# Performance work log

Measured on AMD Instinct MI355X. Metric: run time of the kernel, lower is better.

The kernel has to match this reference:

```python
import jax, jax.numpy as jnp
import numpy as np

B, N, D, H, O = 4096, 128, 64, 256, 128  # batch, memory_size, memory_dim, controller_dim, output_size


def setup_inputs() -> dict:
    key = jax.random.key(0)
    ks = jax.random.split(key, 20)
    s = 0.05
    inp = {
        "x": jax.random.normal(ks[0], (B, O), jnp.float32),
        "memory": jax.random.normal(ks[1], (B, N, D), jnp.float32),
        "h": jax.random.normal(ks[2], (B, H), jnp.float32),
        "c": jax.random.normal(ks[3], (B, H), jnp.float32),
        # LSTMCell params (torch layout: gates ordered i, f, g, o; input = x||read_vec of width O+D)
        "W_ih": jax.random.normal(ks[4], (4 * H, O + D), jnp.float32) * s,
        "W_hh": jax.random.normal(ks[5], (4 * H, H), jnp.float32) * s,
        "b_ih": jax.random.normal(ks[6], (4 * H,), jnp.float32) * s,
        "b_hh": jax.random.normal(ks[7], (4 * H,), jnp.float32) * s,
        "W_read": jax.random.normal(ks[8], (N, H), jnp.float32) * s,
        "b_read": jax.random.normal(ks[9], (N,), jnp.float32) * s,
        "W_write": jax.random.normal(ks[10], (N, H), jnp.float32) * s,
        "b_write": jax.random.normal(ks[11], (N,), jnp.float32) * s,
        "W_erase": jax.random.normal(ks[12], (D, H), jnp.float32) * s,
        "b_erase": jax.random.normal(ks[13], (D,), jnp.float32) * s,
        "W_add": jax.random.normal(ks[14], (D, H), jnp.float32) * s,
        "b_add": jax.random.normal(ks[15], (D,), jnp.float32) * s,
        "W_out": jax.random.normal(ks[16], (O, H + D), jnp.float32) * s,
        "b_out": jax.random.normal(ks[17], (O,), jnp.float32) * s,
    }
    return inp


def reference(x, memory, h, c, W_ih, W_hh, b_ih, b_hh, W_read, b_read,
              W_write, b_write, W_erase, b_erase, W_add, b_add, W_out, b_out):
    # read: softmax attention over memory rows, addressed by previous hidden state
    read_w = jax.nn.softmax(h @ W_read.T + b_read, axis=-1)          # [B, N]
    read_vec = jnp.einsum("bn,bnd->bd", read_w, memory)               # [B, D]

    # LSTMCell step (torch gate order: i, f, g, o)
    ctrl_in = jnp.concatenate([x, read_vec], axis=-1)                 # [B, O+D]
    gates = ctrl_in @ W_ih.T + b_ih + h @ W_hh.T + b_hh               # [B, 4H]
    i, f, g, o = jnp.split(gates, 4, axis=-1)
    i, f, o = jax.nn.sigmoid(i), jax.nn.sigmoid(f), jax.nn.sigmoid(o)
    g = jnp.tanh(g)
    c_new = f * c + i * g
    h_new = o * jnp.tanh(c_new)

    # write: outer-product erase/add update
    write_w = jax.nn.softmax(h_new @ W_write.T + b_write, axis=-1)    # [B, N]
    erase = jax.nn.sigmoid(h_new @ W_erase.T + b_erase)               # [B, D]
    add = jnp.tanh(h_new @ W_add.T + b_add)                           # [B, D]
    ww = write_w[:, :, None]                                          # [B, N, 1]
    mem_new = memory * (1.0 - ww * erase[:, None, :]) + ww * add[:, None, :]

    out = jnp.concatenate([h_new, read_vec], axis=-1) @ W_out.T + b_out  # [B, O]
    return (out, mem_new, h_new, c_new)
```

## Files before the change

### kernel.cpp

```cpp
#include <hip/hip_runtime.h>
#include <math.h>


typedef __attribute__((ext_vector_type(8))) short bf16x8;
typedef __attribute__((ext_vector_type(4))) float f32x4;
typedef __attribute__((ext_vector_type(4))) unsigned short us4;

#define MFMA16(a, b, c) __builtin_amdgcn_mfma_f32_16x16x32_bf16(a, b, c, 0, 0, 0)
#define GLL16(gp, lp) __builtin_amdgcn_global_load_lds( \
    (const __attribute__((address_space(1))) void*)(gp), \
    (__attribute__((address_space(3))) void*)(lp), 16, 0, 0)
#define SW(row, s) ((s) ^ ((row) & 3))

__device__ __forceinline__ float sigf(float v) { return 1.f / (1.f + __expf(-v)); }

__device__ __forceinline__ unsigned short f2bf(float f) {
    unsigned u = __builtin_bit_cast(unsigned, f);
    u = (u + 0x7FFFu + ((u >> 16) & 1u)) >> 16;
    return (unsigned short)u;
}

__device__ __forceinline__ int swA8(int r, int c) {
    return r * 320 + (c & ~31) + ((((c >> 3) & 3) ^ (r & 3)) << 3) + (c & 7);
}

__global__ __launch_bounds__(256) void kA_scores(
    const float* __restrict__ h, const float* __restrict__ Wr,
    const float* __restrict__ br, float* __restrict__ read_w)
{
    __shared__ unsigned short As[16 * 32];
    __shared__ unsigned short Bs[128 * 32];
    __shared__ float sc[16][128];

    int t = threadIdx.x;
    int wid = t >> 6, lane = t & 63;
    int cl = lane & 15, ks = lane >> 4;
    int b0 = blockIdx.x * 16;

    int aOff = cl * 32 + SW(cl, ks) * 8;
    int bOff[4];
#pragma unroll
    for (int f = 0; f < 4; ++f) {
        int br_ = (wid * 4 + f) * 16 + cl;
        bOff[f] = br_ * 32 + SW(br_, ks) * 8;
    }
    f32x4 acc[4] = {};
    for (int kc = 0; kc < 8; ++kc) {
        __syncthreads();
        {
            int row = t >> 4, k0 = (t & 15) * 2;
            float2 hv = *(const float2*)(h + (size_t)(b0 + row) * 256 + kc * 32 + k0);
            unsigned pk = (unsigned)f2bf(hv.x) | ((unsigned)f2bf(hv.y) << 16);
            *(unsigned*)(As + row * 32 + SW(row, k0 >> 3) * 8 + (k0 & 7)) = pk;
        }
        {
            int row = t >> 1, k0 = (t & 1) * 16;
            const float4* wp = (const float4*)(Wr + (size_t)row * 256 + kc * 32 + k0);
            float4 w0 = wp[0], w1 = wp[1], w2 = wp[2], w3 = wp[3];
            us4 p0 = { f2bf(w0.x), f2bf(w0.y), f2bf(w0.z), f2bf(w0.w) };
            us4 p1 = { f2bf(w1.x), f2bf(w1.y), f2bf(w1.z), f2bf(w1.w) };
            us4 p2 = { f2bf(w2.x), f2bf(w2.y), f2bf(w2.z), f2bf(w2.w) };
            us4 p3 = { f2bf(w3.x), f2bf(w3.y), f2bf(w3.z), f2bf(w3.w) };
            int g0 = k0 >> 3;
            unsigned short* basep = Bs + row * 32;
            *(us4*)(basep + SW(row, g0) * 8)         = p0;
            *(us4*)(basep + SW(row, g0) * 8 + 4)     = p1;
            *(us4*)(basep + SW(row, g0 + 1) * 8)     = p2;
            *(us4*)(basep + SW(row, g0 + 1) * 8 + 4) = p3;
        }
        __syncthreads();
        if (wid < 2) {
            bf16x8 a = *(const bf16x8*)(As + aOff);
#pragma unroll
            for (int f = 0; f < 4; ++f)
                acc[f] = MFMA16(a, *(const bf16x8*)(Bs + bOff[f]), acc[f]);
        }
    }
    if (wid < 2) {
#pragma unroll
        for (int f = 0; f < 4; ++f)
#pragma unroll
            for (int r = 0; r < 4; ++r)
                sc[ks * 4 + r][(wid * 4 + f) * 16 + cl] = acc[f][r];
    }
    __syncthreads();
    {
        int row = t >> 4, l = t & 15;
        float v[8];
#pragma unroll
        for (int j = 0; j < 8; ++j) v[j] = sc[row][l + 16 * j] + br[l + 16 * j];
        float m = v[0];
#pragma unroll
        for (int j = 1; j < 8; ++j) m = fmaxf(m, v[j]);
#pragma unroll
        for (int mk = 8; mk >= 1; mk >>= 1) m = fmaxf(m, __shfl_xor(m, mk));
        float s = 0.f;
#pragma unroll
        for (int j = 0; j < 8; ++j) { v[j] = __expf(v[j] - m); s += v[j]; }
#pragma unroll
        for (int mk = 8; mk >= 1; mk >>= 1) s += __shfl_xor(s, mk);
        float inv = 1.f / s;
#pragma unroll
        for (int j = 0; j < 8; ++j)
            read_w[(size_t)(b0 + row) * 128 + l + 16 * j] = v[j] * inv;
    }
}

__global__ __launch_bounds__(256) void k2_stream_pack(
    const float* __restrict__ mem, const float* __restrict__ read_w,
    const float* __restrict__ x, const float* __restrict__ h,
    const float* __restrict__ Wih, const float* __restrict__ Whh,
    const float* __restrict__ bih, const float* __restrict__ bhh,
    const float* __restrict__ Ww, const float* __restrict__ We,
    const float* __restrict__ Wa, const float* __restrict__ bw,
    const float* __restrict__ be, const float* __restrict__ ba,
    const float* __restrict__ Wo,
    unsigned short* __restrict__ Wg, unsigned short* __restrict__ Wh_b,
    unsigned short* __restrict__ Wo_b, float* __restrict__ bsum,
    float* __restrict__ bh_b, unsigned short* __restrict__ Ag,
    unsigned short* __restrict__ Aout)
{
    __shared__ float part[16][68];
    int t = threadIdx.x;
    int b = blockIdx.x;
    unsigned idx = b * 256 + t;

    if (idx < 458752) {
        int r = idx / 448, cc = idx - r * 448;
        float v = (cc < 192) ? Wih[(size_t)r * 192 + cc] : Whh[(size_t)r * 256 + (cc - 192)];
        Wg[idx] = f2bf(v);
    }
    if (idx < 65536) {
        int r = idx >> 8, cc = idx & 255;
        float v = (r < 128) ? Ww[(size_t)r * 256 + cc]
                : (r < 192) ? We[(size_t)(r - 128) * 256 + cc]
                            : Wa[(size_t)(r - 192) * 256 + cc];
        Wh_b[idx] = f2bf(v);
    }
    if (idx < 40960) Wo_b[idx] = f2bf(Wo[idx]);
    if (idx < 1024)  bsum[idx] = bih[idx] + bhh[idx];
    if (idx < 256)
        bh_b[idx] = (idx < 128) ? bw[idx] : (idx < 192 ? be[idx - 128] : ba[idx - 192]);

    if (t < 96) {
        int j = t;
        float4 v = (j < 32) ? ((const float4*)(x + (size_t)b * 128))[j]
                            : ((const float4*)(h + (size_t)b * 256))[j - 32];
        us4 o = { f2bf(v.x), f2bf(v.y), f2bf(v.z), f2bf(v.w) };
        int col = (j < 32) ? j * 4 : 192 + (j - 32) * 4;
        *(us4*)(Ag + (size_t)b * 448 + col) = o;
    }

    int np = t >> 4, d4 = t & 15;
    const float4* m4 = (const float4*)(mem + (size_t)b * 8192);
    float4 acc = make_float4(0.f, 0.f, 0.f, 0.f);
#pragma unroll
    for (int j = 0; j < 8; ++j) {
        int n = np + 16 * j;
        float w = read_w[(size_t)b * 128 + n];
        float4 mv = m4[t + 256 * j];
        acc.x += w * mv.x; acc.y += w * mv.y; acc.z += w * mv.z; acc.w += w * mv.w;
    }
    part[np][d4 * 4 + 0] = acc.x; part[np][d4 * 4 + 1] = acc.y;
    part[np][d4 * 4 + 2] = acc.z; part[np][d4 * 4 + 3] = acc.w;
    __syncthreads();
    if (t < 64) {
        float s = 0.f;
#pragma unroll
        for (int q = 0; q < 16; ++q) s += part[q][t];
        unsigned short bv = f2bf(s);
        Ag[(size_t)b * 448 + 128 + t] = bv;
        Aout[(size_t)b * 320 + 256 + t] = bv;
    }
}

__global__ __launch_bounds__(256) void kB_gates(
    const unsigned short* __restrict__ Ag, const unsigned short* __restrict__ Wg,
    const float* __restrict__ bsum, const float* __restrict__ c,
    float* __restrict__ h_new, float* __restrict__ c_new,
    unsigned short* __restrict__ Aout)
{
    __shared__ unsigned short As[32 * 64];
    __shared__ unsigned short Bs[256 * 64];
    int t = threadIdx.x;
    int wid = t >> 6, lane = t & 63;
    int cl = lane & 15, ks = lane >> 4;
    int b0 = blockIdx.x * 32;
    int u0 = blockIdx.y * 64;

    int arow = t >> 3, aseg = t & 7;
    const unsigned short* aSrc = Ag + (size_t)(b0 + arow) * 448 + ((aseg ^ (arow & 7)) * 8);
    unsigned short* aDst = As + t * 8;
    const unsigned short* bSrc[8];
    unsigned short* bDst[8];
#pragma unroll
    for (int j = 0; j < 8; ++j) {
        int i = j * 256 + t;
        int rl = i >> 3, seg = i & 7;
        int g = rl >> 6, u = rl & 63;
        bSrc[j] = Wg + (size_t)(g * 256 + u0 + u) * 448 + ((seg ^ (rl & 7)) * 8);
        bDst[j] = Bs + i * 8;
    }

    int aOff[2][2];
#pragma unroll
    for (int rf = 0; rf < 2; ++rf)
#pragma unroll
        for (int kk = 0; kk < 2; ++kk) {
            int mr = rf * 16 + cl;
            aOff[rf][kk] = mr * 64 + (((kk * 4 + ks) ^ (cl & 7)) * 8);
        }
    int bOff[4][2];
#pragma unroll
    for (int g = 0; g < 4; ++g)
#pragma unroll
        for (int kk = 0; kk < 2; ++kk) {
            int br_ = g * 64 + wid * 16 + cl;
            bOff[g][kk] = br_ * 64 + (((kk * 4 + ks) ^ (cl & 7)) * 8);
        }

    f32x4 acc[2][4] = {};
    for (int kc = 0; kc < 7; ++kc) {
        __syncthreads();
        GLL16(aSrc, aDst);
#pragma unroll
        for (int j = 0; j < 8; ++j) GLL16(bSrc[j], bDst[j]);
        aSrc += 64;
#pragma unroll
        for (int j = 0; j < 8; ++j) bSrc[j] += 64;
        __syncthreads();
#pragma unroll
        for (int kk = 0; kk < 2; ++kk) {
            bf16x8 a[2], b[4];
#pragma unroll
            for (int rf = 0; rf < 2; ++rf) a[rf] = *(const bf16x8*)(As + aOff[rf][kk]);
#pragma unroll
            for (int g = 0; g < 4; ++g) b[g] = *(const bf16x8*)(Bs + bOff[g][kk]);
#pragma unroll
            for (int rf = 0; rf < 2; ++rf)
#pragma unroll
                for (int g = 0; g < 4; ++g)
                    acc[rf][g] = MFMA16(a[rf], b[g], acc[rf][g]);
        }
    }

    int unit = u0 + wid * 16 + cl;
    float bi = bsum[unit], bf_ = bsum[256 + unit];
    float bg = bsum[512 + unit], bo_ = bsum[768 + unit];
#pragma unroll
    for (int rf = 0; rf < 2; ++rf) {
#pragma unroll
        for (int r = 0; r < 4; ++r) {
            int row = b0 + rf * 16 + ks * 4 + r;
            float iv = sigf(acc[rf][0][r] + bi);
            float fv = sigf(acc[rf][1][r] + bf_);
            float gv = tanhf(acc[rf][2][r] + bg);
            float ov = sigf(acc[rf][3][r] + bo_);
            float cv = fv * c[(size_t)row * 256 + unit] + iv * gv;
            float hv = ov * tanhf(cv);
            c_new[(size_t)row * 256 + unit] = cv;
            h_new[(size_t)row * 256 + unit] = hv;
            Aout[(size_t)row * 320 + unit] = f2bf(hv);
        }
    }
}

__global__ __launch_bounds__(256) void kC_heads_out(
    const unsigned short* __restrict__ Aout, const unsigned short* __restrict__ Wh_b,
    const unsigned short* __restrict__ Wo_b, const float* __restrict__ bh_b,
    const float* __restrict__ bo, float* __restrict__ write_w,
    float* __restrict__ erase, float* __restrict__ addv, float* __restrict__ outp)
{
    __shared__ unsigned short As8[8 * 320];
    __shared__ unsigned short Bh[256 * 32];
    __shared__ unsigned short Bo[128 * 32];
    __shared__ float sc8[8][256];

    int t = threadIdx.x;
    int wid = t >> 6, lane = t & 63;
    int cl = lane & 15, ks = lane >> 4;
    int r0 = blockIdx.x * 8;

    for (int i = t; i < 640; i += 256) {
        int row = i / 80, c4 = (i - row * 80) * 4;
        us4 v = *(const us4*)(Aout + (size_t)(r0 + row) * 320 + c4);
        *(us4*)(As8 + swA8(row, c4)) = v;
    }

    const unsigned short* bhSrc[4];
    unsigned short* bhDst[4];
#pragma unroll
    for (int j = 0; j < 4; ++j) {
        int rl = (j * 256 + t) >> 2;
        bhSrc[j] = Wh_b + (size_t)rl * 256 + SW(rl, t & 3) * 8;
        bhDst[j] = Bh + (j * 256 + wid * 64) * 8;
    }
    const unsigned short* boSrc[2];
    unsigned short* boDst[2];
#pragma unroll
    for (int j = 0; j < 2; ++j) {
        int rj = j * 64 + (t >> 2);
        boSrc[j] = Wo_b + (size_t)rj * 320 + SW(rj, t & 3) * 8;
        boDst[j] = Bo + j * 2048 + wid * 512;
    }

    int bOffH[4], bOffO[2];
#pragma unroll
    for (int j = 0; j < 4; ++j) { int br_ = (wid + 4 * j) * 16 + cl; bOffH[j] = br_ * 32 + SW(br_, ks) * 8; }
#pragma unroll
    for (int j = 0; j < 2; ++j) { int br_ = (wid + 4 * j) * 16 + cl; bOffO[j] = br_ * 32 + SW(br_, ks) * 8; }

    f32x4 accH[4] = {};
    f32x4 accO[2] = {};
    for (int kc = 0; kc < 10; ++kc) {
        __syncthreads();
        if (kc < 8) {
            GLL16(bhSrc[0], bhDst[0]); GLL16(bhSrc[1], bhDst[1]);
            GLL16(bhSrc[2], bhDst[2]); GLL16(bhSrc[3], bhDst[3]);
#pragma unroll
            for (int j = 0; j < 4; ++j) bhSrc[j] += 32;
        }
        GLL16(boSrc[0], boDst[0]); GLL16(boSrc[1], boDst[1]);
#pragma unroll
        for (int j = 0; j < 2; ++j) boSrc[j] += 32;
        __syncthreads();
        bf16x8 a = *(const bf16x8*)(As8 + swA8(cl & 7, kc * 32 + ks * 8));
        if (kc < 8) {
#pragma unroll
            for (int j = 0; j < 4; ++j)
                accH[j] = MFMA16(a, *(const bf16x8*)(Bh + bOffH[j]), accH[j]);
        }
#pragma unroll
        for (int j = 0; j < 2; ++j)
            accO[j] = MFMA16(a, *(const bf16x8*)(Bo + bOffO[j]), accO[j]);
    }

    if (ks < 2) {
#pragma unroll
        for (int j = 0; j < 4; ++j) {
            int col = (wid + 4 * j) * 16 + cl;
            float bb = bh_b[col];
#pragma unroll
            for (int r = 0; r < 4; ++r) sc8[ks * 4 + r][col] = accH[j][r] + bb;
        }
#pragma unroll
        for (int j = 0; j < 2; ++j) {
            int ocol = (wid + 4 * j) * 16 + cl;
            float bb = bo[ocol];
#pragma unroll
            for (int r = 0; r < 4; ++r)
                outp[(size_t)(r0 + ks * 4 + r) * 128 + ocol] = accO[j][r] + bb;
        }
    }
    __syncthreads();

    if (t < 128) {
        int row = t >> 4, l = t & 15;
        float v[8];
#pragma unroll
        for (int j = 0; j < 8; ++j) v[j] = sc8[row][l + 16 * j];
        float m = v[0];
#pragma unroll
        for (int j = 1; j < 8; ++j) m = fmaxf(m, v[j]);
#pragma unroll
        for (int mk = 8; mk >= 1; mk >>= 1) m = fmaxf(m, __shfl_xor(m, mk));
        float s = 0.f;
#pragma unroll
        for (int j = 0; j < 8; ++j) { v[j] = __expf(v[j] - m); s += v[j]; }
#pragma unroll
        for (int mk = 8; mk >= 1; mk >>= 1) s += __shfl_xor(s, mk);
        float inv = 1.f / s;
        int row_g = r0 + row;
#pragma unroll
        for (int j = 0; j < 8; ++j)
            write_w[(size_t)row_g * 128 + l + 16 * j] = v[j] * inv;
#pragma unroll
        for (int j = 0; j < 4; ++j)
            erase[(size_t)row_g * 64 + l + 16 * j] = sigf(sc8[row][128 + l + 16 * j]);
#pragma unroll
        for (int j = 0; j < 4; ++j)
            addv[(size_t)row_g * 64 + l + 16 * j] = tanhf(sc8[row][192 + l + 16 * j]);
    }
}

__global__ __launch_bounds__(256) void k5_mem_update(
    const float* __restrict__ mem, const float* __restrict__ write_w,
    const float* __restrict__ erase, const float* __restrict__ addv,
    float* __restrict__ mem_new)
{
    int t = threadIdx.x; int b = blockIdx.x;
    int np = t >> 4, d0 = (t & 15) * 4;
    const f32x4* m4 = (const f32x4*)(mem + (size_t)b * 8192);
    f32x4* o4 = (f32x4*)(mem_new + (size_t)b * 8192);
    f32x4 e4 = *(const f32x4*)(erase + (size_t)b * 64 + d0);
    f32x4 a4 = *(const f32x4*)(addv + (size_t)b * 64 + d0);
#pragma unroll
    for (int j = 0; j < 8; ++j) {
        int n = np + 16 * j;
        float w = write_w[(size_t)b * 128 + n];
        f32x4 m = m4[t + 256 * j];
        f32x4 r;
        r[0] = m[0] * (1.f - w * e4[0]) + w * a4[0];
        r[1] = m[1] * (1.f - w * e4[1]) + w * a4[1];
        r[2] = m[2] * (1.f - w * e4[2]) + w * a4[2];
        r[3] = m[3] * (1.f - w * e4[3]) + w * a4[3];
        __builtin_nontemporal_store(r, &o4[t + 256 * j]);
    }
}

extern "C" void kernel_launch(void* const* d_in, const int* in_sizes, int n_in,
                              void* d_out, int out_size, void* d_ws, size_t ws_size,
                              hipStream_t stream)
{
    const float* x    = (const float*)d_in[0];
    const float* mem  = (const float*)d_in[1];
    const float* h    = (const float*)d_in[2];
    const float* c    = (const float*)d_in[3];
    const float* Wih  = (const float*)d_in[4];
    const float* Whh  = (const float*)d_in[5];
    const float* bih  = (const float*)d_in[6];
    const float* bhh  = (const float*)d_in[7];
    const float* Wr   = (const float*)d_in[8];
    const float* br   = (const float*)d_in[9];
    const float* Ww   = (const float*)d_in[10];
    const float* bw   = (const float*)d_in[11];
    const float* We   = (const float*)d_in[12];
    const float* be   = (const float*)d_in[13];
    const float* Wa   = (const float*)d_in[14];
    const float* ba   = (const float*)d_in[15];
    const float* Wo   = (const float*)d_in[16];
    const float* bo   = (const float*)d_in[17];

    float* out     = (float*)d_out;
    float* mem_new = out + 524288;
    float* h_new   = out + 34078720;
    float* c_new   = out + 35127296;

    float* ws      = (float*)d_ws;
    float* read_w  = ws;
    float* write_w = ws + 524288;
    float* erase   = ws + 1048576;
    float* addv    = ws + 1310720;
    float* bsum    = ws + 1572864;
    float* bh_b    = ws + 1573888;
    unsigned short* ub   = (unsigned short*)(ws + 1574144);
    unsigned short* Ag   = ub;
    unsigned short* Aout = ub + 1835008;
    unsigned short* Wg   = ub + 3145728;
    unsigned short* Wh_b = ub + 3604480;
    unsigned short* Wo_b = ub + 3670016;

    kA_scores<<<256, 256, 0, stream>>>(h, Wr, br, read_w);
    k2_stream_pack<<<4096, 256, 0, stream>>>(mem, read_w, x, h, Wih, Whh, bih, bhh,
                                             Ww, We, Wa, bw, be, ba, Wo,
                                             Wg, Wh_b, Wo_b, bsum, bh_b, Ag, Aout);
    kB_gates<<<dim3(128, 4), 256, 0, stream>>>(Ag, Wg, bsum, c, h_new, c_new, Aout);
    kC_heads_out<<<512, 256, 0, stream>>>(Aout, Wh_b, Wo_b, bh_b, bo,
                                          write_w, erase, addv, out);
    k5_mem_update<<<4096, 256, 0, stream>>>(mem, write_w, erase, addv, mem_new);
}
```

Baseline: 103.3 us.

## Fuse read-score GEMV and softmax into memory streaming kernel

```diff
diff --git a/kernel.cpp b/kernel.cpp
--- a/kernel.cpp
+++ b/kernel.cpp
@@ -24,93 +24,12 @@
     return r * 320 + (c & ~31) + ((((c >> 3) & 3) ^ (r & 3)) << 3) + (c & 7);
 }
 
-__global__ __launch_bounds__(256) void kA_scores(
-    const float* __restrict__ h, const float* __restrict__ Wr,
-    const float* __restrict__ br, float* __restrict__ read_w)
-{
-    __shared__ unsigned short As[16 * 32];
-    __shared__ unsigned short Bs[128 * 32];
-    __shared__ float sc[16][128];
-
-    int t = threadIdx.x;
-    int wid = t >> 6, lane = t & 63;
-    int cl = lane & 15, ks = lane >> 4;
-    int b0 = blockIdx.x * 16;
-
-    int aOff = cl * 32 + SW(cl, ks) * 8;
-    int bOff[4];
-#pragma unroll
-    for (int f = 0; f < 4; ++f) {
-        int br_ = (wid * 4 + f) * 16 + cl;
-        bOff[f] = br_ * 32 + SW(br_, ks) * 8;
-    }
-    f32x4 acc[4] = {};
-    for (int kc = 0; kc < 8; ++kc) {
-        __syncthreads();
-        {
-            int row = t >> 4, k0 = (t & 15) * 2;
-            float2 hv = *(const float2*)(h + (size_t)(b0 + row) * 256 + kc * 32 + k0);
-            unsigned pk = (unsigned)f2bf(hv.x) | ((unsigned)f2bf(hv.y) << 16);
-            *(unsigned*)(As + row * 32 + SW(row, k0 >> 3) * 8 + (k0 & 7)) = pk;
-        }
-        {
-            int row = t >> 1, k0 = (t & 1) * 16;
-            const float4* wp = (const float4*)(Wr + (size_t)row * 256 + kc * 32 + k0);
-            float4 w0 = wp[0], w1 = wp[1], w2 = wp[2], w3 = wp[3];
-            us4 p0 = { f2bf(w0.x), f2bf(w0.y), f2bf(w0.z), f2bf(w0.w) };
-            us4 p1 = { f2bf(w1.x), f2bf(w1.y), f2bf(w1.z), f2bf(w1.w) };
-            us4 p2 = { f2bf(w2.x), f2bf(w2.y), f2bf(w2.z), f2bf(w2.w) };
-            us4 p3 = { f2bf(w3.x), f2bf(w3.y), f2bf(w3.z), f2bf(w3.w) };
-            int g0 = k0 >> 3;
-            unsigned short* basep = Bs + row * 32;
-            *(us4*)(basep + SW(row, g0) * 8)         = p0;
-            *(us4*)(basep + SW(row, g0) * 8 + 4)     = p1;
-            *(us4*)(basep + SW(row, g0 + 1) * 8)     = p2;
-            *(us4*)(basep + SW(row, g0 + 1) * 8 + 4) = p3;
-        }
-        __syncthreads();
-        if (wid < 2) {
-            bf16x8 a = *(const bf16x8*)(As + aOff);
-#pragma unroll
-            for (int f = 0; f < 4; ++f)
-                acc[f] = MFMA16(a, *(const bf16x8*)(Bs + bOff[f]), acc[f]);
-        }
-    }
-    if (wid < 2) {
-#pragma unroll
-        for (int f = 0; f < 4; ++f)
-#pragma unroll
-            for (int r = 0; r < 4; ++r)
-                sc[ks * 4 + r][(wid * 4 + f) * 16 + cl] = acc[f][r];
-    }
-    __syncthreads();
-    {
-        int row = t >> 4, l = t & 15;
-        float v[8];
-#pragma unroll
-        for (int j = 0; j < 8; ++j) v[j] = sc[row][l + 16 * j] + br[l + 16 * j];
-        float m = v[0];
-#pragma unroll
-        for (int j = 1; j < 8; ++j) m = fmaxf(m, v[j]);
-#pragma unroll
-        for (int mk = 8; mk >= 1; mk >>= 1) m = fmaxf(m, __shfl_xor(m, mk));
-        float s = 0.f;
-#pragma unroll
-        for (int j = 0; j < 8; ++j) { v[j] = __expf(v[j] - m); s += v[j]; }
-#pragma unroll
-        for (int mk = 8; mk >= 1; mk >>= 1) s += __shfl_xor(s, mk);
-        float inv = 1.f / s;
-#pragma unroll
-        for (int j = 0; j < 8; ++j)
-            read_w[(size_t)(b0 + row) * 128 + l + 16 * j] = v[j] * inv;
-    }
-}
-
 __global__ __launch_bounds__(256) void k2_stream_pack(
-    const float* __restrict__ mem, const float* __restrict__ read_w,
+    const float* __restrict__ mem,
     const float* __restrict__ x, const float* __restrict__ h,
     const float* __restrict__ Wih, const float* __restrict__ Whh,
     const float* __restrict__ bih, const float* __restrict__ bhh,
+    const float* __restrict__ Wr, const float* __restrict__ br,
     const float* __restrict__ Ww, const float* __restrict__ We,
     const float* __restrict__ Wa, const float* __restrict__ bw,
     const float* __restrict__ be, const float* __restrict__ ba,
@@ -121,6 +40,8 @@
     unsigned short* __restrict__ Aout)
 {
     __shared__ float part[16][68];
+    __shared__ float scr[128];
+    __shared__ float wL[128];
     int t = threadIdx.x;
     int b = blockIdx.x;
     unsigned idx = b * 256 + t;
@@ -151,13 +72,42 @@
         *(us4*)(Ag + (size_t)b * 448 + col) = o;
     }
 
+    {
+        int w = t >> 6, l = t & 63;
+        float4 hv = ((const float4*)(h + (size_t)b * 256))[l];
+#pragma unroll 4
+        for (int i = 0; i < 32; ++i) {
+            int n = w * 32 + i;
+            float4 wv = ((const float4*)(Wr + (size_t)n * 256))[l];
+            float s = wv.x * hv.x + wv.y * hv.y + wv.z * hv.z + wv.w * hv.w;
+#pragma unroll
+            for (int mk = 32; mk >= 1; mk >>= 1) s += __shfl_xor(s, mk);
+            if (l == 0) scr[n] = s + br[n];
+        }
+    }
+    __syncthreads();
+    if (t < 64) {
+        float v0 = scr[t], v1 = scr[t + 64];
+        float m = fmaxf(v0, v1);
+#pragma unroll
+        for (int mk = 32; mk >= 1; mk >>= 1) m = fmaxf(m, __shfl_xor(m, mk));
+        float e0 = __expf(v0 - m), e1 = __expf(v1 - m);
+        float s = e0 + e1;
+#pragma unroll
+        for (int mk = 32; mk >= 1; mk >>= 1) s += __shfl_xor(s, mk);
+        float inv = 1.f / s;
+        wL[t] = e0 * inv;
+        wL[t + 64] = e1 * inv;
+    }
+    __syncthreads();
+
     int np = t >> 4, d4 = t & 15;
     const float4* m4 = (const float4*)(mem + (size_t)b * 8192);
     float4 acc = make_float4(0.f, 0.f, 0.f, 0.f);
 #pragma unroll
     for (int j = 0; j < 8; ++j) {
         int n = np + 16 * j;
-        float w = read_w[(size_t)b * 128 + n];
+        float w = wL[n];
         float4 mv = m4[t + 256 * j];
         acc.x += w * mv.x; acc.y += w * mv.y; acc.z += w * mv.z; acc.w += w * mv.w;
     }
@@ -437,7 +387,6 @@
     float* c_new   = out + 35127296;
 
     float* ws      = (float*)d_ws;
-    float* read_w  = ws;
     float* write_w = ws + 524288;
     float* erase   = ws + 1048576;
     float* addv    = ws + 1310720;
@@ -450,8 +399,7 @@
     unsigned short* Wh_b = ub + 3604480;
     unsigned short* Wo_b = ub + 3670016;
 
-    kA_scores<<<256, 256, 0, stream>>>(h, Wr, br, read_w);
-    k2_stream_pack<<<4096, 256, 0, stream>>>(mem, read_w, x, h, Wih, Whh, bih, bhh,
+    k2_stream_pack<<<4096, 256, 0, stream>>>(mem, x, h, Wih, Whh, bih, bhh, Wr, br,
                                              Ww, We, Wa, bw, be, ba, Wo,
                                              Wg, Wh_b, Wo_b, bsum, bh_b, Ag, Aout);
     kB_gates<<<dim3(128, 4), 256, 0, stream>>>(Ag, Wg, bsum, c, h_new, c_new, Aout);
```

After: 128.6 us. 1.25x slower.
